# Kernel tuning notes

Measured on AMD Instinct MI355X. Metric: run time of the kernel, lower is better.

## Reference

```python
import jax, jax.numpy as jnp
import numpy as np
from bisect import bisect

# hyperparameters (from init_kwargs)
DELTA = 1e-4
GAMMA = 0.1
UTILITY_SCALE = -0.01
PRIORITY_RAIL = 0.5
LOSS_BALANCE = 1.0
ALPHA_ELU = 1.0
ENTROPY_THRESHOLDS = [0, 10, 50]
ENTROPY_LEVELS = [0.0, 0.05, 0.1, 1.0]
MASK_LEVEL = 10000.0

N = 512


def setup_inputs() -> dict:
    key = jax.random.key(0)
    k1, k2, k3, k4 = jax.random.split(key, 4)
    soft_adj = jax.random.uniform(k1, (N, N), dtype=jnp.float32)
    # original adjacency is a binary {0,1} float mask
    original_adj = (jax.random.uniform(k2, (N, N)) > 0.5).astype(jnp.float32)
    distances = jax.random.uniform(k3, (N, N), dtype=jnp.float32) * 100.0
    flow = jax.random.uniform(k4, (N, N), dtype=jnp.float32) * 10.0
    epoch = 20  # python int, selects entropy penalty level via bisect
    return {"soft_adj": soft_adj, "original_adj": original_adj,
            "distances": distances, "flow": flow, "epoch": epoch}


def _shortest_path(soft_adj, distances):
    """Soft (softmin via logsumexp) Floyd-Warshall all-pairs shortest path."""
    W = distances / (soft_adj + DELTA)          # [N, N] effective edge weights
    n = W.shape[0]
    w0 = W * (1.0 - jnp.eye(n, dtype=W.dtype))  # zero diagonal

    def step(w, k):
        # softmin(w, w[:,k,None] + w[None,k,:]) without materializing a stack
        path_through_k = w[:, k][:, None] + w[k, :][None, :]
        w_new = -GAMMA * jnp.logaddexp(-w / GAMMA, -path_through_k / GAMMA)
        return w_new, None

    w_dist, _ = jax.lax.scan(step, w0, jnp.arange(n))
    return w_dist


def reference(soft_adj, original_adj, distances, flow, epoch):
    loss_cost = jnp.sum(soft_adj * distances)

    shortest_paths = _shortest_path(soft_adj, distances)

    exp_ut_rail = jnp.exp(UTILITY_SCALE * shortest_paths * PRIORITY_RAIL)
    exp_ut_base = jnp.exp(UTILITY_SCALE * distances)
    choice_matrix = exp_ut_rail / (exp_ut_rail + exp_ut_base)
    distance_saved = distances - PRIORITY_RAIL * shortest_paths
    utility_gain = flow * choice_matrix * distance_saved
    utility_gain = jax.nn.elu(utility_gain, alpha=ALPHA_ELU) + ALPHA_ELU

    inverse_soft = jnp.eye(soft_adj.shape[0], dtype=soft_adj.dtype) - soft_adj
    entropy_loss = jnp.sum(jnp.square(soft_adj * inverse_soft))
    entropy_scale = ENTROPY_LEVELS[bisect(ENTROPY_THRESHOLDS, epoch)]

    mask_loss = jnp.sum(soft_adj * (1.0 - original_adj))

    return (loss_cost
            + LOSS_BALANCE * jnp.sum(utility_gain)
            + entropy_loss * entropy_scale
            + MASK_LEVEL * mask_loss)
```

## Files before the change

kernel.cpp:

```cpp
#include <hip/hip_runtime.h>
#include <math.h>

#define NN 512
#define KP 64
#define NPANEL 8
#define NTHR 256
#define NBLK 256
#define TRUNITS (448 * 112)

#define D_   0
#define V_   4160
#define B2_  8320
#define UB_  12672
#define SB_  17024
#define H_   21376
#define LDSN 25728

__device__ __forceinline__ float einit(const float* s, const float* dI, int i, int j) {
  float w = dI[i * NN + j] / (s[i * NN + j] + 1e-4f);
  if (i == j) w = 0.f;
  return expf(-10.f * w);
}

__global__ __launch_bounds__(NTHR) void fw_p0(
    const float* __restrict__ s, const float* __restrict__ dI,
    float* __restrict__ Cs, float* __restrict__ Rs, float* __restrict__ out) {
  __shared__ __align__(16) float lds[LDSN];
  const int blk = blockIdx.x, tid = threadIdx.x;
  const bool isC = (blk < 16);
  const int sb = (blk >> 1) & 7;
  const int h = blk & 1;
  const int sOff = sb * KP;
  const bool haveSl = (sb != 0);
  if (blk == 0 && tid == 0) out[0] = 0.f;

  for (int e = tid; e < 4096; e += NTHR) {
    const int a = e >> 6, b = e & 63;
    lds[D_ + a * 65 + b] = einit(s, dI, a, b);
  }
  if (haveSl) {
    if (isC) {
      for (int e = tid; e < 2048; e += NTHR) {
        const int a = 32 * h + (e >> 6), b = e & 63;
        lds[V_ + a * 65 + b] = einit(s, dI, sOff + a, b);
      }
    } else {
      for (int e = tid; e < 2048; e += NTHR) {
        const int m = e >> 5, j = 32 * h + (e & 31);
        lds[V_ + j * 65 + m] = einit(s, dI, m, sOff + j);
      }
    }
  }
  __syncthreads();

  if (tid < 64) {
    float x[64];
    if (isC) {
#pragma unroll
      for (int a = 0; a < 64; ++a) x[a] = lds[D_ + a * 65 + tid];
    } else {
#pragma unroll
      for (int a = 0; a < 64; ++a) x[a] = lds[D_ + tid * 65 + a];
    }
#pragma unroll
    for (int m = 0; m < 64; ++m) {
      const float xm = x[m];
      lds[H_ + m * 68 + tid] = xm;
#pragma unroll
      for (int a = 0; a < 64; ++a) {
        const int sa = __builtin_amdgcn_readlane(__float_as_int(x[a]), m);
        x[a] += __int_as_float(sa) * xm;
      }
    }
  } else if (tid < 192) {
    if (!haveSl) {
      for (int e = tid - 64; e < 4096; e += 128) {
        const int a = e >> 6, b = e & 63;
        lds[V_ + a * 65 + b] = isC ? lds[D_ + a * 65 + b] : lds[D_ + b * 65 + a];
      }
    }
  }
  __syncthreads();

  for (int cch = 0; cch < 4; ++cch) {
    const int mb = cch * 16;
    if (cch > 0 && tid < 128) {
      const int r = 32 * h + (tid & 31);
      const int g = tid >> 5;
      const int m0c = mb + 4 * g;
      const int vb = V_ + r * 65;
      float a0 = lds[vb + m0c + 0], a1 = lds[vb + m0c + 1];
      float a2 = lds[vb + m0c + 2], a3 = lds[vb + m0c + 3];
      for (int mp = 0; mp < mb; ++mp) {
        const float vr = lds[vb + mp];
        const float4 u4 = *(const float4*)&lds[H_ + mp * 68 + m0c];
        a0 += vr * u4.x; a1 += vr * u4.y; a2 += vr * u4.z; a3 += vr * u4.w;
      }
      lds[vb + m0c + 0] = a0; lds[vb + m0c + 1] = a1;
      lds[vb + m0c + 2] = a2; lds[vb + m0c + 3] = a3;
    }
    __syncthreads();
    if (tid < 32) {
      const int r = 32 * h + tid;
      const int vb = V_ + r * 65 + mb;
      float v[16];
#pragma unroll
      for (int u2 = 0; u2 < 16; ++u2) v[u2] = lds[vb + u2];
#pragma unroll
      for (int mp = 0; mp < 15; ++mp) {
        const float vmp = v[mp];
#pragma unroll
        for (int m2 = mp + 1; m2 < 16; ++m2)
          v[m2] += vmp * lds[H_ + (mb + mp) * 68 + (mb + m2)];
      }
#pragma unroll
      for (int u2 = 0; u2 < 16; ++u2) lds[vb + u2] = v[u2];
    }
    __syncthreads();
  }

  if (isC) {
    for (int e = tid; e < 2048; e += NTHR) {
      const int a = 32 * h + (e >> 6), b = e & 63;
      Cs[(size_t)(sOff + a) * KP + b] = lds[V_ + a * 65 + b];
    }
  } else {
    for (int e = tid; e < 2048; e += NTHR) {
      const int m = e >> 5, j = 32 * h + (e & 31);
      Rs[(size_t)m * NN + (sOff + j)] = lds[V_ + j * 65 + m];
    }
  }
}

__global__ __launch_bounds__(NTHR) void fw_phase(
    const float* __restrict__ s, const float* __restrict__ dI,
    float* __restrict__ E, float* __restrict__ Cs, float* __restrict__ Rs,
    int p) {
  __shared__ __align__(16) float lds[LDSN];
  const int blk = blockIdx.x, tid = threadIdx.x;
  const int k0 = p * KP;
  const float* Cprev = Cs + (size_t)(p - 1) * (NN * KP);
  const float* Rprev = Rs + (size_t)(p - 1) * (KP * NN);

  if (blk >= 32) {
    const int gt = (blk - 32) * NTHR + tid;
    if (gt >= TRUNITS) return;
    const int ii = gt / 112;
    const int jj = gt - ii * 112;
    const int i = (ii < k0) ? ii : ii + KP;
    const int j = ((jj < (p << 4)) ? jj : jj + 16) << 2;
    const int idx = i * NN + j;
    float4 acc;
    if (p == 1) {
      acc.x = einit(s, dI, i, j + 0);
      acc.y = einit(s, dI, i, j + 1);
      acc.z = einit(s, dI, i, j + 2);
      acc.w = einit(s, dI, i, j + 3);
    } else {
      acc = *(const float4*)(E + idx);
    }
    const float* crow = Cprev + (size_t)i * KP;
    const float* rcol = Rprev + j;
#pragma unroll 8
    for (int r = 0; r < KP; ++r) {
      const float cv = crow[r];
      const float4 rv = *(const float4*)(rcol + (size_t)r * NN);
      acc.x += cv * rv.x; acc.y += cv * rv.y;
      acc.z += cv * rv.z; acc.w += cv * rv.w;
    }
    *(float4*)(E + idx) = acc;
    return;
  }

  const bool isC = (blk < 16);
  const int sb = (blk >> 1) & 7;
  const int h = blk & 1;
  const int sOff = sb * KP;
  const bool haveSl = (sb != p);

  const int r0d = (tid >> 4) << 2, m0d = (tid & 15) << 2;
  float4 epre[4];
  if (p == 1) {
#pragma unroll
    for (int i2 = 0; i2 < 4; ++i2) {
      epre[i2].x = einit(s, dI, k0 + r0d + i2, k0 + m0d + 0);
      epre[i2].y = einit(s, dI, k0 + r0d + i2, k0 + m0d + 1);
      epre[i2].z = einit(s, dI, k0 + r0d + i2, k0 + m0d + 2);
      epre[i2].w = einit(s, dI, k0 + r0d + i2, k0 + m0d + 3);
    }
  } else {
#pragma unroll
    for (int i2 = 0; i2 < 4; ++i2)
      epre[i2] = *(const float4*)(E + (size_t)(k0 + r0d + i2) * NN + (k0 + m0d));
  }

#pragma unroll
  for (int k = 0; k < 4; ++k) {
    const int e4 = tid + k * NTHR;
    const int a = e4 >> 4, b4 = (e4 & 15) << 2;
    *(float4*)&lds[B2_ + a * 68 + b4] =
        *(const float4*)(Cprev + (size_t)(k0 + a) * KP + b4);
    *(float4*)&lds[UB_ + a * 68 + b4] =
        *(const float4*)(Rprev + (size_t)a * NN + (k0 + b4));
    if (haveSl) {
      if (isC)
        *(float4*)&lds[SB_ + a * 68 + b4] =
            *(const float4*)(Cprev + (size_t)(sOff + a) * KP + b4);
      else
        *(float4*)&lds[SB_ + a * 68 + b4] =
            *(const float4*)(Rprev + (size_t)a * NN + (sOff + b4));
    }
  }
  __syncthreads();

  {
    float acc[4][4];
#pragma unroll
    for (int i2 = 0; i2 < 4; ++i2) {
      acc[i2][0] = epre[i2].x; acc[i2][1] = epre[i2].y;
      acc[i2][2] = epre[i2].z; acc[i2][3] = epre[i2].w;
    }
    for (int rr = 0; rr < KP; ++rr) {
      const float4 b4 = *(const float4*)&lds[UB_ + rr * 68 + m0d];
#pragma unroll
      for (int i2 = 0; i2 < 4; ++i2) {
        const float av = lds[B2_ + (r0d + i2) * 68 + rr];
        acc[i2][0] += av * b4.x; acc[i2][1] += av * b4.y;
        acc[i2][2] += av * b4.z; acc[i2][3] += av * b4.w;
      }
    }
#pragma unroll
    for (int i2 = 0; i2 < 4; ++i2)
#pragma unroll
      for (int j2 = 0; j2 < 4; ++j2)
        lds[D_ + (r0d + i2) * 65 + (m0d + j2)] = acc[i2][j2];
  }
  __syncthreads();

  if (tid < 64) {
    float x[64];
    if (isC) {
#pragma unroll
      for (int a = 0; a < 64; ++a) x[a] = lds[D_ + a * 65 + tid];
    } else {
#pragma unroll
      for (int a = 0; a < 64; ++a) x[a] = lds[D_ + tid * 65 + a];
    }
#pragma unroll
    for (int m = 0; m < 64; ++m) {
      const float xm = x[m];
      lds[H_ + m * 68 + tid] = xm;
#pragma unroll
      for (int a = 0; a < 64; ++a) {
        const int sa = __builtin_amdgcn_readlane(__float_as_int(x[a]), m);
        x[a] += __int_as_float(sa) * xm;
      }
    }
  } else if (tid < 192) {
    const int tt = tid - 64;
    if (haveSl) {
      float acc[4][4];
      if (isC) {
        const int r0 = 32 * h + ((tt >> 4) << 2);
        const int m0 = (tt & 15) << 2;
        if (p == 1) {
#pragma unroll
          for (int i2 = 0; i2 < 4; ++i2) {
            acc[i2][0] = einit(s, dI, sOff + r0 + i2, k0 + m0 + 0);
            acc[i2][1] = einit(s, dI, sOff + r0 + i2, k0 + m0 + 1);
            acc[i2][2] = einit(s, dI, sOff + r0 + i2, k0 + m0 + 2);
            acc[i2][3] = einit(s, dI, sOff + r0 + i2, k0 + m0 + 3);
          }
        } else {
#pragma unroll
          for (int i2 = 0; i2 < 4; ++i2) {
            const float4 ev = *(const float4*)(E + (size_t)(sOff + r0 + i2) * NN + (k0 + m0));
            acc[i2][0] = ev.x; acc[i2][1] = ev.y; acc[i2][2] = ev.z; acc[i2][3] = ev.w;
          }
        }
        for (int rr = 0; rr < KP; ++rr) {
          const float4 b4 = *(const float4*)&lds[UB_ + rr * 68 + m0];
#pragma unroll
          for (int i2 = 0; i2 < 4; ++i2) {
            const float av = lds[SB_ + (r0 + i2) * 68 + rr];
            acc[i2][0] += av * b4.x; acc[i2][1] += av * b4.y;
            acc[i2][2] += av * b4.z; acc[i2][3] += av * b4.w;
          }
        }
#pragma unroll
        for (int i2 = 0; i2 < 4; ++i2) {
          *(float4*)(E + (size_t)(sOff + r0 + i2) * NN + (k0 + m0)) =
              make_float4(acc[i2][0], acc[i2][1], acc[i2][2], acc[i2][3]);
#pragma unroll
          for (int j2 = 0; j2 < 4; ++j2)
            lds[V_ + (r0 + i2) * 65 + (m0 + j2)] = acc[i2][j2];
        }
      } else {
        const int r0 = (tt & 15) << 2;
        const int c0 = 32 * h + ((tt >> 4) << 2);
        if (p == 1) {
#pragma unroll
          for (int i2 = 0; i2 < 4; ++i2) {
            acc[i2][0] = einit(s, dI, k0 + r0 + i2, sOff + c0 + 0);
            acc[i2][1] = einit(s, dI, k0 + r0 + i2, sOff + c0 + 1);
            acc[i2][2] = einit(s, dI, k0 + r0 + i2, sOff + c0 + 2);
            acc[i2][3] = einit(s, dI, k0 + r0 + i2, sOff + c0 + 3);
          }
        } else {
#pragma unroll
          for (int i2 = 0; i2 < 4; ++i2) {
            const float4 ev = *(const float4*)(E + (size_t)(k0 + r0 + i2) * NN + (sOff + c0));
            acc[i2][0] = ev.x; acc[i2][1] = ev.y; acc[i2][2] = ev.z; acc[i2][3] = ev.w;
          }
        }
        for (int rr = 0; rr < KP; ++rr) {
          const float4 b4 = *(const float4*)&lds[SB_ + rr * 68 + c0];
#pragma unroll
          for (int i2 = 0; i2 < 4; ++i2) {
            const float av = lds[B2_ + (r0 + i2) * 68 + rr];
            acc[i2][0] += av * b4.x; acc[i2][1] += av * b4.y;
            acc[i2][2] += av * b4.z; acc[i2][3] += av * b4.w;
          }
        }
#pragma unroll
        for (int i2 = 0; i2 < 4; ++i2) {
          *(float4*)(E + (size_t)(k0 + r0 + i2) * NN + (sOff + c0)) =
              make_float4(acc[i2][0], acc[i2][1], acc[i2][2], acc[i2][3]);
#pragma unroll
          for (int j2 = 0; j2 < 4; ++j2)
            lds[V_ + (c0 + j2) * 65 + (r0 + i2)] = acc[i2][j2];
        }
      }
    } else {
      for (int e = tt; e < 4096; e += 128) {
        const int a = e >> 6, b = e & 63;
        lds[V_ + a * 65 + b] = isC ? lds[D_ + a * 65 + b] : lds[D_ + b * 65 + a];
      }
    }
  } else {
    if (p == 1 && !haveSl && isC) {
      for (int e = 2048 * h + (tid - 192); e < 2048 * (h + 1); e += 64) {
        const int a = e >> 6, b = e & 63;
        E[(size_t)(k0 + a) * NN + (k0 + b)] = einit(s, dI, k0 + a, k0 + b);
      }
    }
  }
  __syncthreads();

  for (int cch = 0; cch < 4; ++cch) {
    const int mb = cch * 16;
    if (cch > 0 && tid < 128) {
      const int r = 32 * h + (tid & 31);
      const int g = tid >> 5;
      const int m0c = mb + 4 * g;
      const int vb = V_ + r * 65;
      float a0 = lds[vb + m0c + 0], a1 = lds[vb + m0c + 1];
      float a2 = lds[vb + m0c + 2], a3 = lds[vb + m0c + 3];
      for (int mp = 0; mp < mb; ++mp) {
        const float vr = lds[vb + mp];
        const float4 u4 = *(const float4*)&lds[H_ + mp * 68 + m0c];
        a0 += vr * u4.x; a1 += vr * u4.y; a2 += vr * u4.z; a3 += vr * u4.w;
      }
      lds[vb + m0c + 0] = a0; lds[vb + m0c + 1] = a1;
      lds[vb + m0c + 2] = a2; lds[vb + m0c + 3] = a3;
    }
    __syncthreads();
    if (tid < 32) {
      const int r = 32 * h + tid;
      const int vb = V_ + r * 65 + mb;
      float v[16];
#pragma unroll
      for (int u2 = 0; u2 < 16; ++u2) v[u2] = lds[vb + u2];
#pragma unroll
      for (int mp = 0; mp < 15; ++mp) {
        const float vmp = v[mp];
#pragma unroll
        for (int m2 = mp + 1; m2 < 16; ++m2)
          v[m2] += vmp * lds[H_ + (mb + mp) * 68 + (mb + m2)];
      }
#pragma unroll
      for (int u2 = 0; u2 < 16; ++u2) lds[vb + u2] = v[u2];
    }
    __syncthreads();
  }

  float* Cp = Cs + (size_t)p * (NN * KP);
  float* Rp = Rs + (size_t)p * (KP * NN);
  if (isC) {
    for (int e = tid; e < 2048; e += NTHR) {
      const int a = 32 * h + (e >> 6), b = e & 63;
      Cp[(size_t)(sOff + a) * KP + b] = lds[V_ + a * 65 + b];
    }
  } else {
    for (int e = tid; e < 2048; e += NTHR) {
      const int m = e >> 5, j = 32 * h + (e & 31);
      Rp[(size_t)m * NN + (sOff + j)] = lds[V_ + j * 65 + m];
    }
  }
}

__device__ __forceinline__ float loss_elem(float Ev, float sv, float ov,
                                           float dv, float fv, int i, int j,
                                           float esc) {
  const float sp = (Ev > 0.f) ? (-0.1f * logf(Ev)) : 1e9f;
  const float ur = expf(-0.005f * sp);
  const float ub = expf(-0.01f * dv);
  const float choice = ur / (ur + ub);
  const float ug = fv * choice * (dv - 0.5f * sp);
  const float util = (ug > 0.f) ? (ug + 1.f) : expf(ug);
  const float ent = sv * (((i == j) ? 1.f : 0.f) - sv);
  return sv * dv + util + esc * ent * ent + 10000.f * (sv * (1.f - ov));
}

__global__ __launch_bounds__(NTHR) void k_loss(
    const float* __restrict__ s, const float* __restrict__ o,
    const float* __restrict__ dI, const float* __restrict__ f,
    const int* __restrict__ ep, const float* __restrict__ E,
    const float* __restrict__ Cs, const float* __restrict__ Rs,
    float* __restrict__ out) {
  __shared__ float red[NTHR];
  const int tid = threadIdx.x;
  const int g = blockIdx.x * NTHR + tid;
  const int idx0 = g * 4;
  const int i = idx0 >> 9;
  const int j = idx0 & (NN - 1);
  const float* C7 = Cs + (size_t)7 * (NN * KP);
  const float* R7 = Rs + (size_t)7 * (KP * NN);
  float4 acc = *(const float4*)(E + idx0);
  {
    const float* crow = C7 + (size_t)i * KP;
    const float* rcol = R7 + j;
#pragma unroll 8
    for (int r = 0; r < KP; ++r) {
      const float cv = crow[r];
      const float4 rv = *(const float4*)(rcol + (size_t)r * NN);
      acc.x += cv * rv.x; acc.y += cv * rv.y;
      acc.z += cv * rv.z; acc.w += cv * rv.w;
    }
  }
  const int bi = i >> 6, bj = j >> 6;
  if (bi == bj && bi >= 1) {
    const float* cf = Cs + (size_t)(bi - 1) * (NN * KP) + (size_t)i * KP;
    const float* rf = Rs + (size_t)(bi - 1) * (KP * NN) + j;
#pragma unroll 8
    for (int r = 0; r < KP; ++r) {
      const float cv = cf[r];
      const float4 rv = *(const float4*)(rf + (size_t)r * NN);
      acc.x += cv * rv.x; acc.y += cv * rv.y;
      acc.z += cv * rv.z; acc.w += cv * rv.w;
    }
  }
  const float4 sv = *(const float4*)(s + idx0);
  const float4 ov = *(const float4*)(o + idx0);
  const float4 dv = *(const float4*)(dI + idx0);
  const float4 fv = *(const float4*)(f + idx0);
  const int e = ep[0];
  const float esc = (e < 0) ? 0.f : (e < 10) ? 0.05f : (e < 50) ? 0.1f : 1.f;
  float lsum = loss_elem(acc.x, sv.x, ov.x, dv.x, fv.x, i, j + 0, esc)
             + loss_elem(acc.y, sv.y, ov.y, dv.y, fv.y, i, j + 1, esc)
             + loss_elem(acc.z, sv.z, ov.z, dv.z, fv.z, i, j + 2, esc)
             + loss_elem(acc.w, sv.w, ov.w, dv.w, fv.w, i, j + 3, esc);
  red[tid] = lsum;
  __syncthreads();
#pragma unroll
  for (int st = 128; st > 0; st >>= 1) {
    if (tid < st) red[tid] += red[tid + st];
    __syncthreads();
  }
  if (tid == 0) atomicAdd(out, red[0]);
}

extern "C" void kernel_launch(void* const* d_in, const int* in_sizes, int n_in,
                              void* d_out, int out_size, void* d_ws, size_t ws_size,
                              hipStream_t stream) {
  const float* s = (const float*)d_in[0];
  const float* o = (const float*)d_in[1];
  const float* d = (const float*)d_in[2];
  const float* f = (const float*)d_in[3];
  const int* ep = (const int*)d_in[4];

  float* E = (float*)d_ws;
  float* Cs = E + NN * NN;
  float* Rs = Cs + NPANEL * NN * KP;
  float* out = (float*)d_out;

  fw_p0<<<32, NTHR, 0, stream>>>(s, d, Cs, Rs, out);
  for (int p = 1; p < NPANEL; ++p)
    fw_phase<<<NBLK, NTHR, 0, stream>>>(s, d, E, Cs, Rs, p);
  k_loss<<<NBLK, NTHR, 0, stream>>>(s, o, d, f, ep, E, Cs, Rs, out);
}
```

Baseline: 246.8 us.

## Block the diagonal panel factorization into 16-wide sub-blocks overlapped with panel GEMMs

Replaces the single-wavefront 64-step serial diagonal-block elimination with a blocked scheme: 16x16 sub-factorizations, triangular solves for the L and U panels, and a trailing 4x4-tiled update, all spread across more threads. The off-diagonal panel GEMM and the triangular forward substitution are split into halves interleaved with these sub-steps, so they overlap with the diagonal work. Phase 0 is folded into the general phase kernel. The cost targeted is the serial critical path within each phase, paid for with more barriers and more LDS per block.

New measurement: 314.0 us. 1.27x slower.

```diff
diff --git a/kernel.cpp b/kernel.cpp
--- a/kernel.cpp
+++ b/kernel.cpp
@@ -10,11 +10,14 @@
 
 #define D_   0
 #define V_   4160
-#define B2_  8320
-#define UB_  12672
-#define SB_  17024
-#define H_   21376
-#define LDSN 25728
+#define H_   8320
+#define G_   12672
+#define B2_  17024
+#define UB_  21376
+#define SB_  25728
+#define HP_  30080
+#define GP_  30352
+#define LDSN 30624
 
 __device__ __forceinline__ float einit(const float* s, const float* dI, int i, int j) {
   float w = dI[i * NN + j] / (s[i * NN + j] + 1e-4f);
@@ -22,120 +25,10 @@
   return expf(-10.f * w);
 }
 
-__global__ __launch_bounds__(NTHR) void fw_p0(
-    const float* __restrict__ s, const float* __restrict__ dI,
-    float* __restrict__ Cs, float* __restrict__ Rs, float* __restrict__ out) {
-  __shared__ __align__(16) float lds[LDSN];
-  const int blk = blockIdx.x, tid = threadIdx.x;
-  const bool isC = (blk < 16);
-  const int sb = (blk >> 1) & 7;
-  const int h = blk & 1;
-  const int sOff = sb * KP;
-  const bool haveSl = (sb != 0);
-  if (blk == 0 && tid == 0) out[0] = 0.f;
-
-  for (int e = tid; e < 4096; e += NTHR) {
-    const int a = e >> 6, b = e & 63;
-    lds[D_ + a * 65 + b] = einit(s, dI, a, b);
-  }
-  if (haveSl) {
-    if (isC) {
-      for (int e = tid; e < 2048; e += NTHR) {
-        const int a = 32 * h + (e >> 6), b = e & 63;
-        lds[V_ + a * 65 + b] = einit(s, dI, sOff + a, b);
-      }
-    } else {
-      for (int e = tid; e < 2048; e += NTHR) {
-        const int m = e >> 5, j = 32 * h + (e & 31);
-        lds[V_ + j * 65 + m] = einit(s, dI, m, sOff + j);
-      }
-    }
-  }
-  __syncthreads();
-
-  if (tid < 64) {
-    float x[64];
-    if (isC) {
-#pragma unroll
-      for (int a = 0; a < 64; ++a) x[a] = lds[D_ + a * 65 + tid];
-    } else {
-#pragma unroll
-      for (int a = 0; a < 64; ++a) x[a] = lds[D_ + tid * 65 + a];
-    }
-#pragma unroll
-    for (int m = 0; m < 64; ++m) {
-      const float xm = x[m];
-      lds[H_ + m * 68 + tid] = xm;
-#pragma unroll
-      for (int a = 0; a < 64; ++a) {
-        const int sa = __builtin_amdgcn_readlane(__float_as_int(x[a]), m);
-        x[a] += __int_as_float(sa) * xm;
-      }
-    }
-  } else if (tid < 192) {
-    if (!haveSl) {
-      for (int e = tid - 64; e < 4096; e += 128) {
-        const int a = e >> 6, b = e & 63;
-        lds[V_ + a * 65 + b] = isC ? lds[D_ + a * 65 + b] : lds[D_ + b * 65 + a];
-      }
-    }
-  }
-  __syncthreads();
-
-  for (int cch = 0; cch < 4; ++cch) {
-    const int mb = cch * 16;
-    if (cch > 0 && tid < 128) {
-      const int r = 32 * h + (tid & 31);
-      const int g = tid >> 5;
-      const int m0c = mb + 4 * g;
-      const int vb = V_ + r * 65;
-      float a0 = lds[vb + m0c + 0], a1 = lds[vb + m0c + 1];
-      float a2 = lds[vb + m0c + 2], a3 = lds[vb + m0c + 3];
-      for (int mp = 0; mp < mb; ++mp) {
-        const float vr = lds[vb + mp];
-        const float4 u4 = *(const float4*)&lds[H_ + mp * 68 + m0c];
-        a0 += vr * u4.x; a1 += vr * u4.y; a2 += vr * u4.z; a3 += vr * u4.w;
-      }
-      lds[vb + m0c + 0] = a0; lds[vb + m0c + 1] = a1;
-      lds[vb + m0c + 2] = a2; lds[vb + m0c + 3] = a3;
-    }
-    __syncthreads();
-    if (tid < 32) {
-      const int r = 32 * h + tid;
-      const int vb = V_ + r * 65 + mb;
-      float v[16];
-#pragma unroll
-      for (int u2 = 0; u2 < 16; ++u2) v[u2] = lds[vb + u2];
-#pragma unroll
-      for (int mp = 0; mp < 15; ++mp) {
-        const float vmp = v[mp];
-#pragma unroll
-        for (int m2 = mp + 1; m2 < 16; ++m2)
-          v[m2] += vmp * lds[H_ + (mb + mp) * 68 + (mb + m2)];
-      }
-#pragma unroll
-      for (int u2 = 0; u2 < 16; ++u2) lds[vb + u2] = v[u2];
-    }
-    __syncthreads();
-  }
-
-  if (isC) {
-    for (int e = tid; e < 2048; e += NTHR) {
-      const int a = 32 * h + (e >> 6), b = e & 63;
-      Cs[(size_t)(sOff + a) * KP + b] = lds[V_ + a * 65 + b];
-    }
-  } else {
-    for (int e = tid; e < 2048; e += NTHR) {
-      const int m = e >> 5, j = 32 * h + (e & 31);
-      Rs[(size_t)m * NN + (sOff + j)] = lds[V_ + j * 65 + m];
-    }
-  }
-}
-
 __global__ __launch_bounds__(NTHR) void fw_phase(
     const float* __restrict__ s, const float* __restrict__ dI,
     float* __restrict__ E, float* __restrict__ Cs, float* __restrict__ Rs,
-    int p) {
+    float* __restrict__ out, int p) {
   __shared__ __align__(16) float lds[LDSN];
   const int blk = blockIdx.x, tid = threadIdx.x;
   const int k0 = p * KP;
@@ -177,43 +70,48 @@
   const int h = blk & 1;
   const int sOff = sb * KP;
   const bool haveSl = (sb != p);
-
-  const int r0d = (tid >> 4) << 2, m0d = (tid & 15) << 2;
-  float4 epre[4];
-  if (p == 1) {
-#pragma unroll
-    for (int i2 = 0; i2 < 4; ++i2) {
-      epre[i2].x = einit(s, dI, k0 + r0d + i2, k0 + m0d + 0);
-      epre[i2].y = einit(s, dI, k0 + r0d + i2, k0 + m0d + 1);
-      epre[i2].z = einit(s, dI, k0 + r0d + i2, k0 + m0d + 2);
-      epre[i2].w = einit(s, dI, k0 + r0d + i2, k0 + m0d + 3);
+  const int UTb = isC ? H_ : G_;
+
+  if (p == 0) {
+    if (blk == 0 && tid == 0) out[0] = 0.f;
+    for (int e = tid; e < 4096; e += NTHR) {
+      const int a = e >> 6, b = e & 63;
+      lds[D_ + a * 65 + b] = einit(s, dI, a, b);
     }
   } else {
-#pragma unroll
-    for (int i2 = 0; i2 < 4; ++i2)
-      epre[i2] = *(const float4*)(E + (size_t)(k0 + r0d + i2) * NN + (k0 + m0d));
-  }
-
-#pragma unroll
-  for (int k = 0; k < 4; ++k) {
-    const int e4 = tid + k * NTHR;
-    const int a = e4 >> 4, b4 = (e4 & 15) << 2;
-    *(float4*)&lds[B2_ + a * 68 + b4] =
-        *(const float4*)(Cprev + (size_t)(k0 + a) * KP + b4);
-    *(float4*)&lds[UB_ + a * 68 + b4] =
-        *(const float4*)(Rprev + (size_t)a * NN + (k0 + b4));
-    if (haveSl) {
-      if (isC)
-        *(float4*)&lds[SB_ + a * 68 + b4] =
-            *(const float4*)(Cprev + (size_t)(sOff + a) * KP + b4);
-      else
-        *(float4*)&lds[SB_ + a * 68 + b4] =
-            *(const float4*)(Rprev + (size_t)a * NN + (sOff + b4));
-    }
-  }
-  __syncthreads();
-
-  {
+    const int r0d = (tid >> 4) << 2, m0d = (tid & 15) << 2;
+    float4 epre[4];
+    if (p == 1) {
+#pragma unroll
+      for (int i2 = 0; i2 < 4; ++i2) {
+        epre[i2].x = einit(s, dI, k0 + r0d + i2, k0 + m0d + 0);
+        epre[i2].y = einit(s, dI, k0 + r0d + i2, k0 + m0d + 1);
+        epre[i2].z = einit(s, dI, k0 + r0d + i2, k0 + m0d + 2);
+        epre[i2].w = einit(s, dI, k0 + r0d + i2, k0 + m0d + 3);
+      }
+    } else {
+#pragma unroll
+      for (int i2 = 0; i2 < 4; ++i2)
+        epre[i2] = *(const float4*)(E + (size_t)(k0 + r0d + i2) * NN + (k0 + m0d));
+    }
+#pragma unroll
+    for (int k = 0; k < 4; ++k) {
+      const int e4 = tid + k * NTHR;
+      const int a = e4 >> 4, b4 = (e4 & 15) << 2;
+      *(float4*)&lds[B2_ + a * 68 + b4] =
+          *(const float4*)(Cprev + (size_t)(k0 + a) * KP + b4);
+      *(float4*)&lds[UB_ + a * 68 + b4] =
+          *(const float4*)(Rprev + (size_t)a * NN + (k0 + b4));
+      if (haveSl) {
+        if (isC)
+          *(float4*)&lds[SB_ + a * 68 + b4] =
+              *(const float4*)(Cprev + (size_t)(sOff + a) * KP + b4);
+        else
+          *(float4*)&lds[SB_ + a * 68 + b4] =
+              *(const float4*)(Rprev + (size_t)a * NN + (sOff + b4));
+      }
+    }
+    __syncthreads();
     float acc[4][4];
 #pragma unroll
     for (int i2 = 0; i2 < 4; ++i2) {
@@ -237,149 +135,286 @@
   }
   __syncthreads();
 
-  if (tid < 64) {
-    float x[64];
-    if (isC) {
-#pragma unroll
-      for (int a = 0; a < 64; ++a) x[a] = lds[D_ + a * 65 + tid];
+  float sacc[4][4];
+
+  for (int r = 0; r < 4; ++r) {
+    const int b0 = 16 * r;
+    if (tid < 128) {
+      const int lane = tid & 63;
+      if (lane < 16) {
+        const int side = tid >> 6;
+        float x[16];
+#pragma unroll
+        for (int a = 0; a < 16; ++a)
+          x[a] = side ? lds[D_ + (b0 + lane) * 65 + (b0 + a)]
+                      : lds[D_ + (b0 + a) * 65 + (b0 + lane)];
+#pragma unroll
+        for (int m = 0; m < 16; ++m) {
+          const float xm = x[m];
+          lds[(side ? GP_ : HP_) + m * 17 + lane] = xm;
+#pragma unroll
+          for (int a = 0; a < 16; ++a) {
+            const int sa = __builtin_amdgcn_readlane(__float_as_int(x[a]), m);
+            x[a] += __int_as_float(sa) * xm;
+          }
+        }
+      }
     } else {
-#pragma unroll
-      for (int a = 0; a < 64; ++a) x[a] = lds[D_ + tid * 65 + a];
-    }
-#pragma unroll
-    for (int m = 0; m < 64; ++m) {
-      const float xm = x[m];
-      lds[H_ + m * 68 + tid] = xm;
-#pragma unroll
-      for (int a = 0; a < 64; ++a) {
-        const int sa = __builtin_amdgcn_readlane(__float_as_int(x[a]), m);
-        x[a] += __int_as_float(sa) * xm;
-      }
-    }
-  } else if (tid < 192) {
-    const int tt = tid - 64;
-    if (haveSl) {
-      float acc[4][4];
-      if (isC) {
-        const int r0 = 32 * h + ((tt >> 4) << 2);
-        const int m0 = (tt & 15) << 2;
-        if (p == 1) {
-#pragma unroll
-          for (int i2 = 0; i2 < 4; ++i2) {
-            acc[i2][0] = einit(s, dI, sOff + r0 + i2, k0 + m0 + 0);
-            acc[i2][1] = einit(s, dI, sOff + r0 + i2, k0 + m0 + 1);
-            acc[i2][2] = einit(s, dI, sOff + r0 + i2, k0 + m0 + 2);
-            acc[i2][3] = einit(s, dI, sOff + r0 + i2, k0 + m0 + 3);
+      const int tt = tid - 128;
+      if (r == 0) {
+        if (haveSl && p > 0) {
+          if (isC) {
+            const int r0 = 32 * h + ((tt >> 4) << 2);
+            const int m0 = (tt & 15) << 2;
+            if (p == 1) {
+#pragma unroll
+              for (int i2 = 0; i2 < 4; ++i2) {
+                sacc[i2][0] = einit(s, dI, sOff + r0 + i2, k0 + m0 + 0);
+                sacc[i2][1] = einit(s, dI, sOff + r0 + i2, k0 + m0 + 1);
+                sacc[i2][2] = einit(s, dI, sOff + r0 + i2, k0 + m0 + 2);
+                sacc[i2][3] = einit(s, dI, sOff + r0 + i2, k0 + m0 + 3);
+              }
+            } else {
+#pragma unroll
+              for (int i2 = 0; i2 < 4; ++i2) {
+                const float4 ev = *(const float4*)(E + (size_t)(sOff + r0 + i2) * NN + (k0 + m0));
+                sacc[i2][0] = ev.x; sacc[i2][1] = ev.y;
+                sacc[i2][2] = ev.z; sacc[i2][3] = ev.w;
+              }
+            }
+            for (int rr = 0; rr < 32; ++rr) {
+              const float4 b4 = *(const float4*)&lds[UB_ + rr * 68 + m0];
+#pragma unroll
+              for (int i2 = 0; i2 < 4; ++i2) {
+                const float av = lds[SB_ + (r0 + i2) * 68 + rr];
+                sacc[i2][0] += av * b4.x; sacc[i2][1] += av * b4.y;
+                sacc[i2][2] += av * b4.z; sacc[i2][3] += av * b4.w;
+              }
+            }
+          } else {
+            const int r0 = (tt & 15) << 2;
+            const int c0 = 32 * h + ((tt >> 4) << 2);
+            if (p == 1) {
+#pragma unroll
+              for (int i2 = 0; i2 < 4; ++i2) {
+                sacc[i2][0] = einit(s, dI, k0 + r0 + i2, sOff + c0 + 0);
+                sacc[i2][1] = einit(s, dI, k0 + r0 + i2, sOff + c0 + 1);
+                sacc[i2][2] = einit(s, dI, k0 + r0 + i2, sOff + c0 + 2);
+                sacc[i2][3] = einit(s, dI, k0 + r0 + i2, sOff + c0 + 3);
+              }
+            } else {
+#pragma unroll
+              for (int i2 = 0; i2 < 4; ++i2) {
+                const float4 ev = *(const float4*)(E + (size_t)(k0 + r0 + i2) * NN + (sOff + c0));
+                sacc[i2][0] = ev.x; sacc[i2][1] = ev.y;
+                sacc[i2][2] = ev.z; sacc[i2][3] = ev.w;
+              }
+            }
+            for (int rr = 0; rr < 32; ++rr) {
+              const float4 b4 = *(const float4*)&lds[SB_ + rr * 68 + c0];
+#pragma unroll
+              for (int i2 = 0; i2 < 4; ++i2) {
+                const float av = lds[B2_ + (r0 + i2) * 68 + rr];
+                sacc[i2][0] += av * b4.x; sacc[i2][1] += av * b4.y;
+                sacc[i2][2] += av * b4.z; sacc[i2][3] += av * b4.w;
+              }
+            }
+          }
+        } else if (haveSl) {
+          for (int e = tt; e < 1024; e += 128) {
+            if (isC) {
+              const int a = 32 * h + (e >> 6), b = e & 63;
+              lds[V_ + a * 65 + b] = einit(s, dI, sOff + a, b);
+            } else {
+              const int j = 32 * h + (e >> 6), m = e & 63;
+              lds[V_ + j * 65 + m] = einit(s, dI, m, sOff + j);
+            }
           }
         } else {
-#pragma unroll
-          for (int i2 = 0; i2 < 4; ++i2) {
-            const float4 ev = *(const float4*)(E + (size_t)(sOff + r0 + i2) * NN + (k0 + m0));
-            acc[i2][0] = ev.x; acc[i2][1] = ev.y; acc[i2][2] = ev.z; acc[i2][3] = ev.w;
-          }
-        }
-        for (int rr = 0; rr < KP; ++rr) {
-          const float4 b4 = *(const float4*)&lds[UB_ + rr * 68 + m0];
-#pragma unroll
-          for (int i2 = 0; i2 < 4; ++i2) {
-            const float av = lds[SB_ + (r0 + i2) * 68 + rr];
-            acc[i2][0] += av * b4.x; acc[i2][1] += av * b4.y;
-            acc[i2][2] += av * b4.z; acc[i2][3] += av * b4.w;
-          }
-        }
-#pragma unroll
-        for (int i2 = 0; i2 < 4; ++i2) {
-          *(float4*)(E + (size_t)(sOff + r0 + i2) * NN + (k0 + m0)) =
-              make_float4(acc[i2][0], acc[i2][1], acc[i2][2], acc[i2][3]);
-#pragma unroll
-          for (int j2 = 0; j2 < 4; ++j2)
-            lds[V_ + (r0 + i2) * 65 + (m0 + j2)] = acc[i2][j2];
+          for (int e = tt; e < 1024; e += 128) {
+            const int a = 32 * h + (e >> 6), b = e & 63;
+            lds[V_ + a * 65 + b] = isC ? lds[D_ + a * 65 + b]
+                                       : lds[D_ + b * 65 + a];
+          }
+        }
+      } else if (tt < 32) {
+        const int c = r - 1;
+        const int row = 32 * h + tt;
+        const int vb = V_ + row * 65 + 16 * c;
+        float v[16];
+#pragma unroll
+        for (int u = 0; u < 16; ++u) v[u] = lds[vb + u];
+#pragma unroll
+        for (int mp = 0; mp < 15; ++mp) {
+          const float vmp = v[mp];
+#pragma unroll
+          for (int m2 = mp + 1; m2 < 16; ++m2)
+            v[m2] += vmp * lds[UTb + (16 * c + mp) * 68 + (16 * c + m2)];
+        }
+#pragma unroll
+        for (int u = 0; u < 16; ++u) lds[vb + u] = v[u];
+      }
+    }
+    __syncthreads();
+
+    if (tid < 64) {
+      float v[16];
+#pragma unroll
+      for (int m = 0; m < 16; ++m) v[m] = lds[D_ + (b0 + m) * 65 + tid];
+#pragma unroll
+      for (int m = 1; m < 16; ++m) {
+#pragma unroll
+        for (int q = 0; q < m; ++q)
+          v[m] += lds[GP_ + q * 17 + m] * v[q];
+      }
+#pragma unroll
+      for (int m = 0; m < 16; ++m) lds[H_ + (b0 + m) * 68 + tid] = v[m];
+    } else if (tid < 128) {
+      const int a = tid - 64;
+      float w[16];
+#pragma unroll
+      for (int q = 0; q < 16; ++q) w[q] = lds[D_ + a * 65 + (b0 + q)];
+#pragma unroll
+      for (int q = 1; q < 16; ++q) {
+#pragma unroll
+        for (int q2 = 0; q2 < q; ++q2)
+          w[q] += lds[HP_ + q2 * 17 + q] * w[q2];
+      }
+#pragma unroll
+      for (int q = 0; q < 16; ++q) lds[G_ + (b0 + q) * 68 + a] = w[q];
+    } else {
+      const int tt = tid - 128;
+      if (r == 0) {
+        if (haveSl && p > 0) {
+          if (isC) {
+            const int r0 = 32 * h + ((tt >> 4) << 2);
+            const int m0 = (tt & 15) << 2;
+            for (int rr = 32; rr < 64; ++rr) {
+              const float4 b4 = *(const float4*)&lds[UB_ + rr * 68 + m0];
+#pragma unroll
+              for (int i2 = 0; i2 < 4; ++i2) {
+                const float av = lds[SB_ + (r0 + i2) * 68 + rr];
+                sacc[i2][0] += av * b4.x; sacc[i2][1] += av * b4.y;
+                sacc[i2][2] += av * b4.z; sacc[i2][3] += av * b4.w;
+              }
+            }
+#pragma unroll
+            for (int i2 = 0; i2 < 4; ++i2) {
+              *(float4*)(E + (size_t)(sOff + r0 + i2) * NN + (k0 + m0)) =
+                  make_float4(sacc[i2][0], sacc[i2][1], sacc[i2][2], sacc[i2][3]);
+#pragma unroll
+              for (int j2 = 0; j2 < 4; ++j2)
+                lds[V_ + (r0 + i2) * 65 + (m0 + j2)] = sacc[i2][j2];
+            }
+          } else {
+            const int r0 = (tt & 15) << 2;
+            const int c0 = 32 * h + ((tt >> 4) << 2);
+            for (int rr = 32; rr < 64; ++rr) {
+              const float4 b4 = *(const float4*)&lds[SB_ + rr * 68 + c0];
+#pragma unroll
+              for (int i2 = 0; i2 < 4; ++i2) {
+                const float av = lds[B2_ + (r0 + i2) * 68 + rr];
+                sacc[i2][0] += av * b4.x; sacc[i2][1] += av * b4.y;
+                sacc[i2][2] += av * b4.z; sacc[i2][3] += av * b4.w;
+              }
+            }
+#pragma unroll
+            for (int i2 = 0; i2 < 4; ++i2) {
+              *(float4*)(E + (size_t)(k0 + r0 + i2) * NN + (sOff + c0)) =
+                  make_float4(sacc[i2][0], sacc[i2][1], sacc[i2][2], sacc[i2][3]);
+#pragma unroll
+              for (int j2 = 0; j2 < 4; ++j2)
+                lds[V_ + (c0 + j2) * 65 + (r0 + i2)] = sacc[i2][j2];
+            }
+          }
+        } else if (haveSl) {
+          for (int e = tt; e < 1024; e += 128) {
+            if (isC) {
+              const int a = 32 * h + 16 + (e >> 6), b = e & 63;
+              lds[V_ + a * 65 + b] = einit(s, dI, sOff + a, b);
+            } else {
+              const int j = 32 * h + 16 + (e >> 6), m = e & 63;
+              lds[V_ + j * 65 + m] = einit(s, dI, m, sOff + j);
+            }
+          }
+        } else {
+          for (int e = tt; e < 1024; e += 128) {
+            const int a = 32 * h + 16 + (e >> 6), b = e & 63;
+            lds[V_ + a * 65 + b] = isC ? lds[D_ + a * 65 + b]
+                                       : lds[D_ + b * 65 + a];
+          }
         }
       } else {
-        const int r0 = (tt & 15) << 2;
-        const int c0 = 32 * h + ((tt >> 4) << 2);
-        if (p == 1) {
-#pragma unroll
-          for (int i2 = 0; i2 < 4; ++i2) {
-            acc[i2][0] = einit(s, dI, k0 + r0 + i2, sOff + c0 + 0);
-            acc[i2][1] = einit(s, dI, k0 + r0 + i2, sOff + c0 + 1);
-            acc[i2][2] = einit(s, dI, k0 + r0 + i2, sOff + c0 + 2);
-            acc[i2][3] = einit(s, dI, k0 + r0 + i2, sOff + c0 + 3);
-          }
-        } else {
-#pragma unroll
-          for (int i2 = 0; i2 < 4; ++i2) {
-            const float4 ev = *(const float4*)(E + (size_t)(k0 + r0 + i2) * NN + (sOff + c0));
-            acc[i2][0] = ev.x; acc[i2][1] = ev.y; acc[i2][2] = ev.z; acc[i2][3] = ev.w;
-          }
-        }
-        for (int rr = 0; rr < KP; ++rr) {
-          const float4 b4 = *(const float4*)&lds[SB_ + rr * 68 + c0];
-#pragma unroll
-          for (int i2 = 0; i2 < 4; ++i2) {
-            const float av = lds[B2_ + (r0 + i2) * 68 + rr];
-            acc[i2][0] += av * b4.x; acc[i2][1] += av * b4.y;
-            acc[i2][2] += av * b4.z; acc[i2][3] += av * b4.w;
-          }
-        }
-#pragma unroll
-        for (int i2 = 0; i2 < 4; ++i2) {
-          *(float4*)(E + (size_t)(k0 + r0 + i2) * NN + (sOff + c0)) =
-              make_float4(acc[i2][0], acc[i2][1], acc[i2][2], acc[i2][3]);
-#pragma unroll
-          for (int j2 = 0; j2 < 4; ++j2)
-            lds[V_ + (c0 + j2) * 65 + (r0 + i2)] = acc[i2][j2];
+        const int row = 32 * h + (tt & 31);
+        const int m0c = 16 * r + 4 * (tt >> 5);
+        const int vb = V_ + row * 65;
+        float a0 = lds[vb + m0c + 0], a1 = lds[vb + m0c + 1];
+        float a2 = lds[vb + m0c + 2], a3 = lds[vb + m0c + 3];
+        const int bound = 16 * r;
+#pragma unroll 8
+        for (int mp = 0; mp < bound; ++mp) {
+          const float vr = lds[vb + mp];
+          const float4 u4 = *(const float4*)&lds[UTb + mp * 68 + m0c];
+          a0 += vr * u4.x; a1 += vr * u4.y; a2 += vr * u4.z; a3 += vr * u4.w;
+        }
+        lds[vb + m0c + 0] = a0; lds[vb + m0c + 1] = a1;
+        lds[vb + m0c + 2] = a2; lds[vb + m0c + 3] = a3;
+      }
+    }
+    __syncthreads();
+
+    if (r < 3) {
+      if (tid < 128) {
+#pragma unroll
+        for (int pass = 0; pass < 2; ++pass) {
+          const int a0 = 4 * (tid >> 4) + 32 * pass;
+          const int c0 = 4 * (tid & 15);
+          float acc[4][4];
+#pragma unroll
+          for (int i2 = 0; i2 < 4; ++i2)
+#pragma unroll
+            for (int j2 = 0; j2 < 4; ++j2)
+              acc[i2][j2] = lds[D_ + (a0 + i2) * 65 + c0 + j2];
+#pragma unroll
+          for (int q = 0; q < 16; ++q) {
+            const float4 h4 = *(const float4*)&lds[H_ + (b0 + q) * 68 + c0];
+#pragma unroll
+            for (int i2 = 0; i2 < 4; ++i2) {
+              const float gv = lds[G_ + (b0 + q) * 68 + (a0 + i2)];
+              acc[i2][0] += gv * h4.x; acc[i2][1] += gv * h4.y;
+              acc[i2][2] += gv * h4.z; acc[i2][3] += gv * h4.w;
+            }
+          }
+#pragma unroll
+          for (int i2 = 0; i2 < 4; ++i2)
+#pragma unroll
+            for (int j2 = 0; j2 < 4; ++j2)
+              lds[D_ + (a0 + i2) * 65 + c0 + j2] = acc[i2][j2];
+        }
+      } else if (r == 0 && p == 1 && !haveSl && isC) {
+        for (int e = 2048 * h + (tid - 128); e < 2048 * (h + 1); e += 128) {
+          const int a = e >> 6, b = e & 63;
+          E[(size_t)(k0 + a) * NN + (k0 + b)] = einit(s, dI, k0 + a, k0 + b);
         }
       }
     } else {
-      for (int e = tt; e < 4096; e += 128) {
-        const int a = e >> 6, b = e & 63;
-        lds[V_ + a * 65 + b] = isC ? lds[D_ + a * 65 + b] : lds[D_ + b * 65 + a];
-      }
-    }
-  } else {
-    if (p == 1 && !haveSl && isC) {
-      for (int e = 2048 * h + (tid - 192); e < 2048 * (h + 1); e += 64) {
-        const int a = e >> 6, b = e & 63;
-        E[(size_t)(k0 + a) * NN + (k0 + b)] = einit(s, dI, k0 + a, k0 + b);
-      }
-    }
-  }
-  __syncthreads();
-
-  for (int cch = 0; cch < 4; ++cch) {
-    const int mb = cch * 16;
-    if (cch > 0 && tid < 128) {
-      const int r = 32 * h + (tid & 31);
-      const int g = tid >> 5;
-      const int m0c = mb + 4 * g;
-      const int vb = V_ + r * 65;
-      float a0 = lds[vb + m0c + 0], a1 = lds[vb + m0c + 1];
-      float a2 = lds[vb + m0c + 2], a3 = lds[vb + m0c + 3];
-      for (int mp = 0; mp < mb; ++mp) {
-        const float vr = lds[vb + mp];
-        const float4 u4 = *(const float4*)&lds[H_ + mp * 68 + m0c];
-        a0 += vr * u4.x; a1 += vr * u4.y; a2 += vr * u4.z; a3 += vr * u4.w;
-      }
-      lds[vb + m0c + 0] = a0; lds[vb + m0c + 1] = a1;
-      lds[vb + m0c + 2] = a2; lds[vb + m0c + 3] = a3;
-    }
-    __syncthreads();
-    if (tid < 32) {
-      const int r = 32 * h + tid;
-      const int vb = V_ + r * 65 + mb;
-      float v[16];
-#pragma unroll
-      for (int u2 = 0; u2 < 16; ++u2) v[u2] = lds[vb + u2];
-#pragma unroll
-      for (int mp = 0; mp < 15; ++mp) {
-        const float vmp = v[mp];
-#pragma unroll
-        for (int m2 = mp + 1; m2 < 16; ++m2)
-          v[m2] += vmp * lds[H_ + (mb + mp) * 68 + (mb + m2)];
-      }
-#pragma unroll
-      for (int u2 = 0; u2 < 16; ++u2) lds[vb + u2] = v[u2];
+      const int tt = tid - 128;
+      if (tid >= 128 && tt < 32) {
+        const int row = 32 * h + tt;
+        const int vb = V_ + row * 65 + 48;
+        float v[16];
+#pragma unroll
+        for (int u = 0; u < 16; ++u) v[u] = lds[vb + u];
+#pragma unroll
+        for (int mp = 0; mp < 15; ++mp) {
+          const float vmp = v[mp];
+#pragma unroll
+          for (int m2 = mp + 1; m2 < 16; ++m2)
+            v[m2] += vmp * lds[UTb + (48 + mp) * 68 + (48 + m2)];
+        }
+#pragma unroll
+        for (int u = 0; u < 16; ++u) lds[vb + u] = v[u];
+      }
     }
     __syncthreads();
   }
@@ -484,8 +519,8 @@
   float* Rs = Cs + NPANEL * NN * KP;
   float* out = (float*)d_out;
 
-  fw_p0<<<32, NTHR, 0, stream>>>(s, d, Cs, Rs, out);
+  fw_phase<<<32, NTHR, 0, stream>>>(s, d, E, Cs, Rs, out, 0);
   for (int p = 1; p < NPANEL; ++p)
-    fw_phase<<<NBLK, NTHR, 0, stream>>>(s, d, E, Cs, Rs, p);
+    fw_phase<<<NBLK, NTHR, 0, stream>>>(s, d, E, Cs, Rs, out, p);
   k_loss<<<NBLK, NTHR, 0, stream>>>(s, o, d, f, ep, E, Cs, Rs, out);
 }
```
